# Kernel optimization log

Measured on AMD Instinct MI355X. Metric: run time of the kernel, lower is better.

Reference implementation:

```python
import jax, jax.numpy as jnp
import numpy as np

N_TOKENS, E, H = 20000, 128, 512
B, T, L = 128, 512, 8


def setup_inputs() -> dict:
    key = jax.random.key(0)
    ks = jax.random.split(key, 9)
    s = 0.02
    return {
        "tokens": jax.random.randint(ks[0], (B, T, L), 0, N_TOKENS),
        "values": jax.random.uniform(ks[1], (B, T, L), dtype=jnp.float32),
        "emb": jax.random.normal(ks[2], (N_TOKENS, E), dtype=jnp.float32) * s,
        "W_ih": jax.random.normal(ks[3], (4 * H, E), dtype=jnp.float32) * s,
        "W_hh": jax.random.normal(ks[4], (4 * H, H), dtype=jnp.float32) * s,
        "b_ih": jnp.zeros((4 * H,), jnp.float32),
        "b_hh": jnp.zeros((4 * H,), jnp.float32),
        "W_out": jax.random.normal(ks[5], (1, H), dtype=jnp.float32) * s,
        "b_out": jnp.zeros((1,), jnp.float32),
    }


def reference(tokens, values, emb, W_ih, W_hh, b_ih, b_hh, W_out, b_out):
    # EmbedTimeseriesW: value-weighted sum of token embeddings per time bin
    e = emb[tokens]                                  # [B,T,L,E]
    x = jnp.einsum('btle,btl->bte', e, values)       # [B,T,E]
    x = jax.nn.relu(x)                               # ReLU (dropout p=0 -> identity)

    xT = jnp.swapaxes(x, 0, 1)                       # [T,B,E]
    b = b_ih + b_hh

    def step(carry, xt):
        h, c = carry
        gates = xt @ W_ih.T + h @ W_hh.T + b         # [B,4H]
        i, f, g, o = jnp.split(gates, 4, axis=-1)    # torch LSTM gate order
        c = jax.nn.sigmoid(f) * c + jax.nn.sigmoid(i) * jnp.tanh(g)
        h = jax.nn.sigmoid(o) * jnp.tanh(c)
        return (h, c), h

    h0 = jnp.zeros((x.shape[0], W_hh.shape[1]), x.dtype)
    (_, _), hs = jax.lax.scan(step, (h0, h0), xT)    # hs: [T,B,H]

    out = jnp.swapaxes(hs, 0, 1) @ W_out.T + b_out   # [B,T,1]
    return out.squeeze(-1)                           # [B,T]
```

## Files before the change

### kernel.cpp

```cpp
#include <hip/hip_runtime.h>
#include <hip/hip_bf16.h>

#define B_   128
#define T_   512
#define L_   8
#define E_   128
#define H_   512

#define BG_   4
#define WPG_  16
#define JW_   32
#define HU64_ (B_ * H_ / 4)

typedef __attribute__((ext_vector_type(8))) short s8v;
typedef __attribute__((ext_vector_type(4))) float f4v;
typedef unsigned long long u64;

__device__ __forceinline__ float bf16u_to_f(unsigned short s) {
  union { unsigned u; float f; } c; c.u = ((unsigned)s) << 16; return c.f;
}
__device__ __forceinline__ u64 llc_load8(const void* p) {
  return __hip_atomic_load((const u64*)p, __ATOMIC_RELAXED, __HIP_MEMORY_SCOPE_AGENT);
}
__device__ __forceinline__ void llc_store8(void* p, u64 v) {
  __hip_atomic_store((u64*)p, v, __ATOMIC_RELAXED, __HIP_MEMORY_SCOPE_AGENT);
}
__device__ __forceinline__ float sigf(float x) { return 1.f / (1.f + __expf(-x)); }

__global__ void embed_kernel(const int* __restrict__ tokens,
                             const float* __restrict__ values,
                             const float* __restrict__ emb,
                             __hip_bfloat16* __restrict__ x_bf) {
  int idx = blockIdx.x * blockDim.x + threadIdx.x;
  int e  = idx & (E_ - 1);
  int bt = idx >> 7;
  int b  = bt >> 9;
  int t  = bt & (T_ - 1);
  const int*   tok = tokens + (size_t)bt * L_;
  const float* val = values + (size_t)bt * L_;
  float acc = 0.f;
#pragma unroll
  for (int l = 0; l < L_; ++l) acc += emb[(size_t)tok[l] * E_ + e] * val[l];
  acc = fmaxf(acc, 0.f);
  x_bf[((size_t)t * B_ + b) * E_ + e] = __float2bfloat16(acc);
}

__device__ __forceinline__ void out_dot_lds(const u64* __restrict__ h_lds,
                                            int t, int bg,
                                            const float* __restrict__ wout_s,
                                            float bout, float* __restrict__ out) {
  const int um = threadIdx.x >> 3;
  const int uj = threadIdx.x & 7;
  const u64* row = h_lds + (size_t)um * 128;
  const float* wr = wout_s + uj * 64;
  float p = 0.f;
#pragma unroll
  for (int j = 0; j < 8; ++j) {
    int pc = ((uj * 8 + j) ^ (um & 7)) * 2;
    u64 qa = row[pc], qb = row[pc + 1];
    p += bf16u_to_f((unsigned short)(qa      )) * wr[j * 8 + 0];
    p += bf16u_to_f((unsigned short)(qa >> 16)) * wr[j * 8 + 1];
    p += bf16u_to_f((unsigned short)(qa >> 32)) * wr[j * 8 + 2];
    p += bf16u_to_f((unsigned short)(qa >> 48)) * wr[j * 8 + 3];
    p += bf16u_to_f((unsigned short)(qb      )) * wr[j * 8 + 4];
    p += bf16u_to_f((unsigned short)(qb >> 16)) * wr[j * 8 + 5];
    p += bf16u_to_f((unsigned short)(qb >> 32)) * wr[j * 8 + 6];
    p += bf16u_to_f((unsigned short)(qb >> 48)) * wr[j * 8 + 7];
  }
  p += __shfl_down(p, 4, 8);
  p += __shfl_down(p, 2, 8);
  p += __shfl_down(p, 1, 8);
  if (uj == 0) out[(size_t)(bg * 32 + um) * T_ + t] = p + bout;
}

__device__ __forceinline__ void out_dot_glb(const u64* __restrict__ h,
                                            int t, int bg,
                                            const float* __restrict__ wout_s,
                                            float bout, float* __restrict__ out) {
  const int um = threadIdx.x >> 3;
  const int uj = threadIdx.x & 7;
  const int b  = bg * 32 + um;
  const u64* hr = h + (size_t)b * 128 + uj * 16;
  const float* wr = wout_s + uj * 64;
  float p = 0.f;
#pragma unroll
  for (int kk = 0; kk < 16; ++kk) {
    u64 q = llc_load8(hr + kk);
    p += bf16u_to_f((unsigned short)(q      )) * wr[kk * 4 + 0];
    p += bf16u_to_f((unsigned short)(q >> 16)) * wr[kk * 4 + 1];
    p += bf16u_to_f((unsigned short)(q >> 32)) * wr[kk * 4 + 2];
    p += bf16u_to_f((unsigned short)(q >> 48)) * wr[kk * 4 + 3];
  }
  p += __shfl_down(p, 4, 8);
  p += __shfl_down(p, 2, 8);
  p += __shfl_down(p, 1, 8);
  if (uj == 0) out[(size_t)b * T_ + t] = p + bout;
}

__global__ void __launch_bounds__(256, 1)
lstm_kernel(const float* __restrict__ W_ih, const float* __restrict__ W_hh,
            const float* __restrict__ b_ih, const float* __restrict__ b_hh,
            const float* __restrict__ W_out, const float* __restrict__ b_out,
            const __hip_bfloat16* __restrict__ x_bf,
            u64* __restrict__ h_base,
            float* __restrict__ out,
            unsigned* __restrict__ bars) {
  __shared__ u64   h_lds[32 * 128];
  __shared__ float gbuf[32][136];
  __shared__ float bias_s[128];
  __shared__ float wout_s[H_];

  const int tid = threadIdx.x;
  const int wg  = blockIdx.x;
  const int bg  = wg >> 4;
  const int g   = wg & (WPG_ - 1);
  const int j0g = g * JW_;

  const int wv   = tid >> 6;
  const int lane = tid & 63;
  const int m16  = lane & 15;
  const int q    = lane >> 4;
  const int sw   = m16 & 7;

  s8v bfrag[2][20];
#pragma unroll
  for (int nt = 0; nt < 2; ++nt) {
    const int r = wv * H_ + j0g + nt * 16 + m16;
    const float* wih_r = W_ih + (size_t)r * E_;
    const float* whh_r = W_hh + (size_t)r * H_;
#pragma unroll
    for (int ks = 0; ks < 20; ++ks) {
      s8v v;
#pragma unroll
      for (int i = 0; i < 8; ++i) {
        int k = ks * 32 + q * 8 + i;
        float w = (k < E_) ? wih_r[k] : whh_r[k - E_];
        __hip_bfloat16 hb = __float2bfloat16(w);
        v[i] = *(short*)&hb;
      }
      bfrag[nt][ks] = v;
    }
  }
  if (tid < 128) {
    int gt = tid >> 5, jl = tid & 31;
    int r = gt * H_ + j0g + jl;
    bias_s[tid] = b_ih[r] + b_hh[r];
  }
  if (g == 0) for (int i = tid; i < H_; i += 256) wout_s[i] = W_out[i];

  const int um = tid >> 3;
  const int jb = (tid & 7) * 4;
  const int ub = bg * 32 + um;
  const int fm = tid >> 3;
  const int fc = tid & 7;
  float cst[4] = {0.f, 0.f, 0.f, 0.f};
  const float bout = b_out[0];
  unsigned* cnt = bars + bg * 64;

  int rp = 2, wp = 0;
  f4v acc[2][2];

  {
    const __hip_bfloat16* xt = x_bf;
    const __hip_bfloat16* ax0 = xt + (size_t)(bg * 32 + m16) * E_ + q * 8;
    const __hip_bfloat16* ax1 = xt + (size_t)(bg * 32 + 16 + m16) * E_ + q * 8;
    f4v z = {0.f, 0.f, 0.f, 0.f};
    acc[0][0] = z; acc[0][1] = z; acc[1][0] = z; acc[1][1] = z;
#pragma unroll
    for (int ks = 0; ks < 4; ++ks) {
      s8v a0 = *(const s8v*)(ax0 + ks * 32);
      s8v a1 = *(const s8v*)(ax1 + ks * 32);
#pragma unroll
      for (int nt = 0; nt < 2; ++nt) {
        acc[0][nt] = __builtin_amdgcn_mfma_f32_16x16x32_bf16(a0, bfrag[nt][ks], acc[0][nt], 0, 0, 0);
        acc[1][nt] = __builtin_amdgcn_mfma_f32_16x16x32_bf16(a1, bfrag[nt][ks], acc[1][nt], 0, 0, 0);
      }
    }
  }
  __syncthreads();

  for (int t = 0; t < T_; ++t) {
    const u64* h_prev = h_base + (size_t)rp * HU64_;
    u64*       h_next = h_base + (size_t)wp * HU64_;

    {
      const u64* src = h_prev + (size_t)(bg * 32 + fm) * 128;
      u64 v[16];
#pragma unroll
      for (int j = 0; j < 8; ++j) {
        int lc = fc + 8 * j;
        v[2 * j]     = llc_load8(src + lc * 2);
        v[2 * j + 1] = llc_load8(src + lc * 2 + 1);
      }
      u64* dst = h_lds + (size_t)fm * 128;
#pragma unroll
      for (int j = 0; j < 8; ++j) {
        int pc = ((fc + 8 * j) ^ (fm & 7)) * 2;
        dst[pc]     = v[2 * j];
        dst[pc + 1] = v[2 * j + 1];
      }
    }
    __syncthreads();

    {
      const u64* al0 = h_lds + (size_t)m16 * 128;
      const u64* al1 = h_lds + (size_t)(16 + m16) * 128;
#pragma unroll
      for (int ks4 = 0; ks4 < 16; ++ks4) {
        int pc = ((ks4 * 4 + q) ^ sw) * 2;
        s8v a0 = *(const s8v*)(al0 + pc);
        s8v a1 = *(const s8v*)(al1 + pc);
#pragma unroll
        for (int nt = 0; nt < 2; ++nt) {
          acc[0][nt] = __builtin_amdgcn_mfma_f32_16x16x32_bf16(a0, bfrag[nt][4 + ks4], acc[0][nt], 0, 0, 0);
          acc[1][nt] = __builtin_amdgcn_mfma_f32_16x16x32_bf16(a1, bfrag[nt][4 + ks4], acc[1][nt], 0, 0, 0);
        }
      }
    }

#pragma unroll
    for (int mt = 0; mt < 2; ++mt)
#pragma unroll
      for (int nt = 0; nt < 2; ++nt)
#pragma unroll
        for (int r = 0; r < 4; ++r)
          gbuf[mt * 16 + q * 4 + r][wv * 32 + nt * 16 + m16] = acc[mt][nt][r];
    __syncthreads();

    {
      u64 packed = 0;
#pragma unroll
      for (int qq = 0; qq < 4; ++qq) {
        int j = jb + qq;
        float gi = gbuf[um][      j] + bias_s[      j];
        float gf = gbuf[um][32  + j] + bias_s[32  + j];
        float gc = gbuf[um][64  + j] + bias_s[64  + j];
        float go = gbuf[um][96  + j] + bias_s[96  + j];
        cst[qq] = sigf(gf) * cst[qq] + sigf(gi) * tanhf(gc);
        float h = sigf(go) * tanhf(cst[qq]);
        __hip_bfloat16 hb = __float2bfloat16(h);
        packed |= (u64)(*(unsigned short*)&hb) << (16 * qq);
      }
      llc_store8(h_next + (size_t)ub * 128 + ((j0g + jb) >> 2), packed);
    }
    __syncthreads();

    if (tid == 0)
      __hip_atomic_fetch_add(cnt, 1u, __ATOMIC_RELAXED, __HIP_MEMORY_SCOPE_AGENT);

    if (g == 0 && t > 0)
      out_dot_lds(h_lds, t - 1, bg, wout_s, bout, out);

    if (t + 1 < T_) {
      const __hip_bfloat16* xt = x_bf + (size_t)(t + 1) * B_ * E_;
      const __hip_bfloat16* ax0 = xt + (size_t)(bg * 32 + m16) * E_ + q * 8;
      const __hip_bfloat16* ax1 = xt + (size_t)(bg * 32 + 16 + m16) * E_ + q * 8;
      f4v z = {0.f, 0.f, 0.f, 0.f};
      acc[0][0] = z; acc[0][1] = z; acc[1][0] = z; acc[1][1] = z;
#pragma unroll
      for (int ks = 0; ks < 4; ++ks) {
        s8v a0 = *(const s8v*)(ax0 + ks * 32);
        s8v a1 = *(const s8v*)(ax1 + ks * 32);
#pragma unroll
        for (int nt = 0; nt < 2; ++nt) {
          acc[0][nt] = __builtin_amdgcn_mfma_f32_16x16x32_bf16(a0, bfrag[nt][ks], acc[0][nt], 0, 0, 0);
          acc[1][nt] = __builtin_amdgcn_mfma_f32_16x16x32_bf16(a1, bfrag[nt][ks], acc[1][nt], 0, 0, 0);
        }
      }
    }

    if (tid == 0) {
      unsigned tgt = (unsigned)(t + 1) * WPG_;
      while (__hip_atomic_load(cnt, __ATOMIC_RELAXED, __HIP_MEMORY_SCOPE_AGENT) < tgt) {
        __builtin_amdgcn_s_sleep(1);
      }
    }
    __syncthreads();

    rp = wp; wp = (wp == 2) ? 0 : wp + 1;
  }

  if (g == 0)
    out_dot_glb(h_base + (size_t)rp * HU64_, T_ - 1, bg, wout_s, bout, out);
}

extern "C" void kernel_launch(void* const* d_in, const int* in_sizes, int n_in,
                              void* d_out, int out_size, void* d_ws, size_t ws_size,
                              hipStream_t stream) {
  const int*   tokens = (const int*)d_in[0];
  const float* values = (const float*)d_in[1];
  const float* emb    = (const float*)d_in[2];
  const float* W_ih   = (const float*)d_in[3];
  const float* W_hh   = (const float*)d_in[4];
  const float* b_ih   = (const float*)d_in[5];
  const float* b_hh   = (const float*)d_in[6];
  const float* W_out  = (const float*)d_in[7];
  const float* b_out  = (const float*)d_in[8];
  float* out = (float*)d_out;

  char* ws = (char*)d_ws;
  __hip_bfloat16* x_bf = (__hip_bfloat16*)ws;
  u64* h_base = (u64*)(ws + (size_t)T_ * B_ * E_ * 2);
  unsigned* bars = (unsigned*)(ws + (size_t)T_ * B_ * E_ * 2
                                  + (size_t)3 * HU64_ * sizeof(u64));

  hipMemsetAsync(h_base, 0, (size_t)3 * HU64_ * sizeof(u64), stream);
  hipMemsetAsync(bars, 0, (size_t)BG_ * 64 * sizeof(unsigned), stream);

  embed_kernel<<<(B_ * T_ * E_) / 256, 256, 0, stream>>>(tokens, values, emb, x_bf);

  lstm_kernel<<<dim3(BG_ * WPG_), dim3(256), 0, stream>>>(
      W_ih, W_hh, b_ih, b_hh, W_out, b_out, x_bf, h_base, out, bars);
}
```

Measured before the change: 2.547 ms.

## Replace atomic counter barrier with per-workgroup flags and fast gate math

Replaces the shared atomic fetch_add counter and single-thread sleep-spin barrier with per-workgroup step flags. A whole wavefront polls 16 flags at the start of the next step, so only one barrier sits on the critical path per step. The next step's input-projection MFMAs move ahead of the gate nonlinearities. Gate math switches to vectorized LDS reads with rcp-based sigmoid/tanh approximations, trading a little accuracy for fewer instructions. Flag publication relies on relaxed atomics after __syncthreads, which may weaken memory ordering.

```diff
diff --git a/kernel.cpp b/kernel.cpp
--- a/kernel.cpp
+++ b/kernel.cpp
@@ -11,6 +11,7 @@
 #define WPG_  16
 #define JW_   32
 #define HU64_ (B_ * H_ / 4)
+#define GSTR  132
 
 typedef __attribute__((ext_vector_type(8))) short s8v;
 typedef __attribute__((ext_vector_type(4))) float f4v;
@@ -25,7 +26,27 @@
 __device__ __forceinline__ void llc_store8(void* p, u64 v) {
   __hip_atomic_store((u64*)p, v, __ATOMIC_RELAXED, __HIP_MEMORY_SCOPE_AGENT);
 }
-__device__ __forceinline__ float sigf(float x) { return 1.f / (1.f + __expf(-x)); }
+__device__ __forceinline__ unsigned llc_load4(const unsigned* p) {
+  return __hip_atomic_load(p, __ATOMIC_RELAXED, __HIP_MEMORY_SCOPE_AGENT);
+}
+__device__ __forceinline__ void llc_store4(unsigned* p, unsigned v) {
+  __hip_atomic_store(p, v, __ATOMIC_RELAXED, __HIP_MEMORY_SCOPE_AGENT);
+}
+__device__ __forceinline__ float sigf(float x) {
+  return __builtin_amdgcn_rcpf(1.f + __expf(-x));
+}
+__device__ __forceinline__ float tanh_f(float x) {
+  return 1.f - 2.f * __builtin_amdgcn_rcpf(1.f + __expf(2.f * x));
+}
+
+__device__ __forceinline__ void wait_flags(const unsigned* flags, unsigned tgt) {
+  const int lane = threadIdx.x & 63;
+  const unsigned* p = flags + (lane & 15);
+  for (;;) {
+    unsigned f = (lane < 16) ? llc_load4(p) : 0xFFFFFFFFu;
+    if (__all((int)(f >= tgt))) break;
+  }
+}
 
 __global__ void embed_kernel(const int* __restrict__ tokens,
                              const float* __restrict__ values,
@@ -105,9 +126,9 @@
             u64* __restrict__ h_base,
             float* __restrict__ out,
             unsigned* __restrict__ bars) {
-  __shared__ u64   h_lds[32 * 128];
-  __shared__ float gbuf[32][136];
-  __shared__ float bias_s[128];
+  __shared__ __align__(16) u64   h_lds[32 * 128];
+  __shared__ __align__(16) float gbuf[32][GSTR];
+  __shared__ __align__(16) float bias_s[128];
   __shared__ float wout_s[H_];
 
   const int tid = threadIdx.x;
@@ -151,19 +172,18 @@
   const int um = tid >> 3;
   const int jb = (tid & 7) * 4;
   const int ub = bg * 32 + um;
-  const int fm = tid >> 3;
   const int fc = tid & 7;
   float cst[4] = {0.f, 0.f, 0.f, 0.f};
   const float bout = b_out[0];
-  unsigned* cnt = bars + bg * 64;
+  unsigned* flags  = bars + bg * 64;
+  unsigned* myflag = flags + g;
 
   int rp = 2, wp = 0;
   f4v acc[2][2];
 
   {
-    const __hip_bfloat16* xt = x_bf;
-    const __hip_bfloat16* ax0 = xt + (size_t)(bg * 32 + m16) * E_ + q * 8;
-    const __hip_bfloat16* ax1 = xt + (size_t)(bg * 32 + 16 + m16) * E_ + q * 8;
+    const __hip_bfloat16* ax0 = x_bf + (size_t)(bg * 32 + m16) * E_ + q * 8;
+    const __hip_bfloat16* ax1 = x_bf + (size_t)(bg * 32 + 16 + m16) * E_ + q * 8;
     f4v z = {0.f, 0.f, 0.f, 0.f};
     acc[0][0] = z; acc[0][1] = z; acc[1][0] = z; acc[1][1] = z;
 #pragma unroll
@@ -183,8 +203,10 @@
     const u64* h_prev = h_base + (size_t)rp * HU64_;
     u64*       h_next = h_base + (size_t)wp * HU64_;
 
+    wait_flags(flags, (unsigned)t);
+
     {
-      const u64* src = h_prev + (size_t)(bg * 32 + fm) * 128;
+      const u64* src = h_prev + (size_t)(bg * 32 + um) * 128;
       u64 v[16];
 #pragma unroll
       for (int j = 0; j < 8; ++j) {
@@ -192,10 +214,10 @@
         v[2 * j]     = llc_load8(src + lc * 2);
         v[2 * j + 1] = llc_load8(src + lc * 2 + 1);
       }
-      u64* dst = h_lds + (size_t)fm * 128;
+      u64* dst = h_lds + (size_t)um * 128;
 #pragma unroll
       for (int j = 0; j < 8; ++j) {
-        int pc = ((fc + 8 * j) ^ (fm & 7)) * 2;
+        int pc = ((fc + 8 * j) ^ (um & 7)) * 2;
         dst[pc]     = v[2 * j];
         dst[pc + 1] = v[2 * j + 1];
       }
@@ -226,30 +248,6 @@
         for (int r = 0; r < 4; ++r)
           gbuf[mt * 16 + q * 4 + r][wv * 32 + nt * 16 + m16] = acc[mt][nt][r];
     __syncthreads();
-
-    {
-      u64 packed = 0;
-#pragma unroll
-      for (int qq = 0; qq < 4; ++qq) {
-        int j = jb + qq;
-        float gi = gbuf[um][      j] + bias_s[      j];
-        float gf = gbuf[um][32  + j] + bias_s[32  + j];
-        float gc = gbuf[um][64  + j] + bias_s[64  + j];
-        float go = gbuf[um][96  + j] + bias_s[96  + j];
-        cst[qq] = sigf(gf) * cst[qq] + sigf(gi) * tanhf(gc);
-        float h = sigf(go) * tanhf(cst[qq]);
-        __hip_bfloat16 hb = __float2bfloat16(h);
-        packed |= (u64)(*(unsigned short*)&hb) << (16 * qq);
-      }
-      llc_store8(h_next + (size_t)ub * 128 + ((j0g + jb) >> 2), packed);
-    }
-    __syncthreads();
-
-    if (tid == 0)
-      __hip_atomic_fetch_add(cnt, 1u, __ATOMIC_RELAXED, __HIP_MEMORY_SCOPE_AGENT);
-
-    if (g == 0 && t > 0)
-      out_dot_lds(h_lds, t - 1, bg, wout_s, bout, out);
 
     if (t + 1 < T_) {
       const __hip_bfloat16* xt = x_bf + (size_t)(t + 1) * B_ * E_;
@@ -269,17 +267,41 @@
       }
     }
 
-    if (tid == 0) {
-      unsigned tgt = (unsigned)(t + 1) * WPG_;
-      while (__hip_atomic_load(cnt, __ATOMIC_RELAXED, __HIP_MEMORY_SCOPE_AGENT) < tgt) {
-        __builtin_amdgcn_s_sleep(1);
-      }
-    }
+    {
+      const float* gr = &gbuf[0][0] + (size_t)um * GSTR;
+      f4v vi = *(const f4v*)(gr + jb);
+      f4v vf = *(const f4v*)(gr + 32 + jb);
+      f4v vg = *(const f4v*)(gr + 64 + jb);
+      f4v vo = *(const f4v*)(gr + 96 + jb);
+      f4v bi = *(const f4v*)(bias_s + jb);
+      f4v bf = *(const f4v*)(bias_s + 32 + jb);
+      f4v bgc = *(const f4v*)(bias_s + 64 + jb);
+      f4v bo = *(const f4v*)(bias_s + 96 + jb);
+      u64 packed = 0;
+#pragma unroll
+      for (int qq = 0; qq < 4; ++qq) {
+        float si = sigf(vi[qq] + bi[qq]);
+        float sf = sigf(vf[qq] + bf[qq]);
+        float tg = tanh_f(vg[qq] + bgc[qq]);
+        float so = sigf(vo[qq] + bo[qq]);
+        cst[qq] = sf * cst[qq] + si * tg;
+        float h = so * tanh_f(cst[qq]);
+        __hip_bfloat16 hb = __float2bfloat16(h);
+        packed |= (u64)(*(unsigned short*)&hb) << (16 * qq);
+      }
+      llc_store8(h_next + (size_t)ub * 128 + ((j0g + jb) >> 2), packed);
+    }
+
+    if (g == 0 && t > 0)
+      out_dot_lds(h_lds, t - 1, bg, wout_s, bout, out);
+
     __syncthreads();
+    if (tid == 0) llc_store4(myflag, (unsigned)(t + 1));
 
     rp = wp; wp = (wp == 2) ? 0 : wp + 1;
   }
 
+  wait_flags(flags, (unsigned)T_);
   if (g == 0)
     out_dot_glb(h_base + (size_t)rp * HU64_, T_ - 1, bg, wout_s, bout, out);
 }
```

New measurement: 2.436 ms. -4.3%, faster.
